# Kernel tuning notes

Measured on AMD Instinct MI355X. Metric: run time of the kernel, lower is better.

The kernel has to match this reference:

```python
import jax, jax.numpy as jnp
import numpy as np

N_NODES = 100000
N_EDGES = 1600000
D_INPUT = 128
D_HIDDEN = 16
N_HEADS = 8
NCLASSES = 40
N_GRAPHS = 64
ALPHA = 0.2  # LeakyReLU negative slope
INIT = 0.01  # GAT_param_init uniform range


def setup_inputs() -> dict:
    key = jax.random.key(0)
    ks = jax.random.split(key, 7)
    x = jax.random.normal(ks[0], (N_NODES, D_INPUT), dtype=jnp.float32)
    edge_idx = jax.random.randint(ks[1], (2, N_EDGES), 0, N_NODES, dtype=jnp.int64)
    batch = jnp.sort(jax.random.randint(ks[2], (N_NODES,), 0, N_GRAPHS, dtype=jnp.int64))
    # layer1: d_input -> n_heads * d_hidden, concat aggregate
    W1 = jax.random.uniform(ks[3], (D_INPUT, N_HEADS * D_HIDDEN), dtype=jnp.float32, minval=-INIT, maxval=INIT)
    a1 = jax.random.uniform(ks[4], (N_HEADS, 2 * D_HIDDEN), dtype=jnp.float32, minval=-INIT, maxval=INIT)
    # layer2: n_heads*d_hidden -> nclasses, 1 head, mean aggregate
    W2 = jax.random.uniform(ks[5], (N_HEADS * D_HIDDEN, NCLASSES), dtype=jnp.float32, minval=-INIT, maxval=INIT)
    a2 = jax.random.uniform(ks[6], (1, 2 * NCLASSES), dtype=jnp.float32, minval=-INIT, maxval=INIT)
    return {"x": x, "W1": W1, "a1": a1, "W2": W2, "a2": a2, "edge_idx": edge_idx, "batch": batch}


def _gat_layer(x, W, a, n_heads, d_out, src, dst, aggregate):
    # x: [N, d_in]; W: [d_in, H*D]; a: [H, 2*D]
    n = x.shape[0]
    Wh = (x @ W).reshape(n, n_heads, d_out)                  # [N, H, D]
    e_src = jnp.einsum('nhd,hd->nh', Wh, a[:, :d_out])       # [N, H]
    e_dst = jnp.einsum('nhd,hd->nh', Wh, a[:, d_out:])       # [N, H]
    e = jax.nn.leaky_relu(e_src[src] + e_dst[dst], ALPHA)    # [E, H]
    # segment softmax over edges sharing the same destination node
    m = jax.ops.segment_max(e, dst, num_segments=n)          # [N, H]
    m = jnp.where(jnp.isfinite(m), m, 0.0)                   # nodes w/o in-edges
    ex = jnp.exp(e - m[dst])
    s = jax.ops.segment_sum(ex, dst, num_segments=n)
    att = ex / (s[dst] + 1e-16)                              # [E, H]
    # weighted scatter-aggregate of neighbor features
    out = jax.ops.segment_sum(att[:, :, None] * Wh[src], dst, num_segments=n)  # [N, H, D]
    if aggregate == 'concat':
        return out.reshape(n, n_heads * d_out)
    return out.mean(axis=1)


def reference(x, W1, a1, W2, a2, edge_idx, batch):
    # eval mode: F.dropout(training=False) is identity
    src, dst = edge_idx[0], edge_idx[1]
    h1 = _gat_layer(x, W1, a1, N_HEADS, D_HIDDEN, src, dst, 'concat')
    h1 = jax.nn.elu(h1)
    h2 = _gat_layer(h1, W2, a2, 1, NCLASSES, src, dst, 'mean')   # [N, nclasses]
    # global_mean_pool over graph ids
    sums = jax.ops.segment_sum(h2, batch, num_segments=N_GRAPHS)
    cnt = jax.ops.segment_sum(jnp.ones((h2.shape[0],), h2.dtype), batch, num_segments=N_GRAPHS)
    return sums / jnp.maximum(cnt, 1.0)[:, None]
```

## Files before the change

### kernel.cpp

```cpp
#include <hip/hip_runtime.h>
#include <hip/hip_bf16.h>

typedef unsigned short u16;
typedef unsigned int   u32;
typedef float f32x2 __attribute__((ext_vector_type(2)));
typedef float f32x4 __attribute__((ext_vector_type(4)));
typedef short bf16x8 __attribute__((ext_vector_type(8)));

static constexpr int NN = 100000;
static constexpr int NE = 1600000;
static constexpr int NG = 64;

static constexpr int BSH   = 8;
static constexpr int NBUCK = 391;
static constexpr int BCAP  = 5120;
static constexpr int PB    = 8;

__device__ __forceinline__ u16 bf16rte(float a) {
  u32 u = __builtin_bit_cast(u32, a);
  u = (u + 0x7FFFu + ((u >> 16) & 1u)) >> 16;
  return (u16)u;
}
__device__ __forceinline__ u32 bf16pair(float a, float b) {
  return (u32)bf16rte(a) | ((u32)bf16rte(b) << 16);
}
__device__ __forceinline__ float bflo(u32 u) { return __builtin_bit_cast(float, u << 16); }
__device__ __forceinline__ float bfhi(u32 u) { return __builtin_bit_cast(float, u & 0xFFFF0000u); }

__device__ __forceinline__ void pkfma(f32x2& a, f32x2 w2, u32 u) {
  f32x2 v;
  v.x = bflo(u); v.y = bfhi(u);
  asm("v_pk_fma_f32 %0, %1, %2, %0" : "+v"(a) : "v"(w2), "v"(v));
}

__global__ void k_prepW(const float* __restrict__ W1, u16* __restrict__ wsTg) {
  const int t = threadIdx.x;
  for (int rep = 0; rep < 64; ++rep) {
    int idx = rep * 256 + t;
    int k = idx >> 7, c = idx & 127;
    float v = W1[idx];
    wsTg[c * 128 + (((k >> 3) ^ (c & 7)) << 3) + (k & 7)] = bf16rte(v);
  }
}

__global__ __launch_bounds__(256) void k_gemm1(
    const float* __restrict__ x, const u16* __restrict__ wsTg, const float* __restrict__ a1,
    u16* __restrict__ Wh1b, float* __restrict__ es1, float* __restrict__ ed1)
{
  __shared__ u16 wsT[128][128];
  __shared__ u16 xsb[64][32];
  const int t = threadIdx.x;
  const int w = t >> 6, l = t & 63;
  const int rowBase = blockIdx.x * 64;

  {
    const uint4* src = (const uint4*)wsTg;
    uint4* dst = (uint4*)&wsT[0][0];
#pragma unroll
    for (int i = 0; i < 8; ++i) dst[t * 8 + i] = src[t * 8 + i];
  }

  f32x4 acc[4][2];
#pragma unroll
  for (int r = 0; r < 4; ++r)
#pragma unroll
    for (int cf = 0; cf < 2; ++cf) acc[r][cf] = (f32x4){0.f, 0.f, 0.f, 0.f};

  const int rr = t >> 2, cg = t & 3;
  const int grow_s = rowBase + rr;

  for (int kk0 = 0; kk0 < 128; kk0 += 32) {
    float4 v0 = make_float4(0.f, 0.f, 0.f, 0.f), v1 = v0;
    if (grow_s < NN) {
      v0 = *(const float4*)(&x[(size_t)grow_s * 128 + kk0 + cg * 8]);
      v1 = *(const float4*)(&x[(size_t)grow_s * 128 + kk0 + cg * 8 + 4]);
    }
    if (kk0) __syncthreads();
    {
      u32 p0 = bf16pair(v0.x, v0.y);
      u32 p1 = bf16pair(v0.z, v0.w);
      u32 p2 = bf16pair(v1.x, v1.y);
      u32 p3 = bf16pair(v1.z, v1.w);
      int sg = cg ^ ((rr >> 1) & 3);
      *(uint4*)(&xsb[rr][sg * 8]) = make_uint4(p0, p1, p2, p3);
    }
    __syncthreads();

    bf16x8 bfr[2];
#pragma unroll
    for (int cf = 0; cf < 2; ++cf) {
      int col = w * 32 + cf * 16 + (l & 15);
      int kg = (kk0 >> 3) + (l >> 4);
      bfr[cf] = *(const bf16x8*)(&wsT[col][(kg ^ (col & 7)) * 8]);
    }
#pragma unroll
    for (int r = 0; r < 4; ++r) {
      int row = r * 16 + (l & 15);
      int kg = l >> 4;
      bf16x8 afr = *(const bf16x8*)(&xsb[row][(kg ^ ((row >> 1) & 3)) * 8]);
#pragma unroll
      for (int cf = 0; cf < 2; ++cf)
        acc[r][cf] = __builtin_amdgcn_mfma_f32_16x16x32_bf16(afr, bfr[cf], acc[r][cf], 0, 0, 0);
    }
  }

  const int cl = l & 15;
  const int rq = l >> 4;
#pragma unroll
  for (int cf = 0; cf < 2; ++cf) {
    const int h = w * 2 + cf;
    const int gcol = w * 32 + cf * 16 + cl;
    const float as = a1[h * 32 + cl];
    const float ad = a1[h * 32 + 16 + cl];
#pragma unroll
    for (int r = 0; r < 4; ++r) {
#pragma unroll
      for (int i = 0; i < 4; ++i) {
        int grow = rowBase + r * 16 + rq * 4 + i;
        float wh = acc[r][cf][i];
        float ps = wh * as, pd = wh * ad;
        ps += __shfl_xor(ps, 1); ps += __shfl_xor(ps, 2);
        ps += __shfl_xor(ps, 4); ps += __shfl_xor(ps, 8);
        pd += __shfl_xor(pd, 1); pd += __shfl_xor(pd, 2);
        pd += __shfl_xor(pd, 4); pd += __shfl_xor(pd, 8);
        if (grow < NN) {
          Wh1b[(size_t)grow * 128 + gcol] = bf16rte(wh);
          if (cl == 0) { es1[grow * 8 + h] = ps; ed1[grow * 8 + h] = pd; }
        }
      }
    }
  }
}

__global__ __launch_bounds__(256) void k_bin(
    const int* __restrict__ src, const int* __restrict__ dst,
    int* __restrict__ cur, u32* __restrict__ ebuf)
{
  __shared__ int lcnt[512];
  __shared__ int goff[NBUCK];
  __shared__ u32 bin[4096];
  const int t = threadIdx.x;
  const int e0 = blockIdx.x * 4096;

  lcnt[t] = 0; lcnt[t + 256] = 0;
  __syncthreads();

  u32 ent[16]; short bb[16], lp[16];
#pragma unroll
  for (int i = 0; i < 16; ++i) {
    int e = e0 + i * 256 + t;
    if (e < NE) {
      int s = src[e], d = dst[e];
      int b = d >> BSH;
      ent[i] = (u32)s | ((u32)(d & 255) << 20);
      bb[i] = (short)b;
      lp[i] = (short)atomicAdd(&lcnt[b], 1);
    } else bb[i] = -1;
  }
  __syncthreads();
  for (int d = 1; d < 512; d <<= 1) {
    int v0 = (t >= d) ? lcnt[t - d] : 0;
    int v1 = (t + 256 >= d) ? lcnt[t + 256 - d] : 0;
    __syncthreads();
    lcnt[t] += v0; lcnt[t + 256] += v1;
    __syncthreads();
  }
  for (int b = t; b < NBUCK; b += 256) {
    int excl = b ? lcnt[b - 1] : 0;
    int cnt = lcnt[b] - excl;
    if (cnt) goff[b] = b * BCAP + atomicAdd(&cur[b], cnt);
  }
#pragma unroll
  for (int i = 0; i < 16; ++i) {
    if (bb[i] >= 0) {
      int excl = bb[i] ? lcnt[bb[i] - 1] : 0;
      bin[excl + lp[i]] = ent[i];
    }
  }
  __syncthreads();
  const int total = lcnt[NBUCK - 1];
  for (int i = t; i < total; i += 256) {
    int lo = 0, hi = NBUCK - 1;
    while (lo < hi) { int mid = (lo + hi) >> 1; if (lcnt[mid] > i) hi = mid; else lo = mid + 1; }
    int excl = lo ? lcnt[lo - 1] : 0;
    int g = goff[lo] + (i - excl);
    if (g < (lo + 1) * BCAP) ebuf[g] = bin[i];
  }
}

__global__ __launch_bounds__(256) void k_sort(
    const int* __restrict__ cur, u32* __restrict__ ebuf,
    int* __restrict__ offs, int* __restrict__ deg)
{
  __shared__ u32 ein[BCAP];
  __shared__ u32 eout[BCAP];
  __shared__ int nd[256];
  __shared__ int ncur[256];
  const int t = threadIdx.x;
  const int b = blockIdx.x;
  const int base = b * BCAP;
  int cnt = cur[b];
  if (cnt > BCAP) cnt = BCAP;
  const int nloc = min(256, NN - (b << BSH));

  for (int i = t; i < cnt; i += 256) ein[i] = ebuf[base + i];
  nd[t] = 0;
  __syncthreads();
  for (int i = t; i < cnt; i += 256) atomicAdd(&nd[ein[i] >> 20], 1);
  __syncthreads();
  const int myCnt = nd[t];
  for (int d = 1; d < 256; d <<= 1) {
    int v = (t >= d) ? nd[t - d] : 0;
    __syncthreads();
    nd[t] += v;
    __syncthreads();
  }
  const int excl = t ? nd[t - 1] : 0;
  ncur[t] = excl;
  if (t < nloc) {
    int node = (b << BSH) + t;
    offs[node] = base + excl;
    deg[node]  = myCnt;
  }
  __syncthreads();
  for (int i = t; i < cnt; i += 256) {
    u32 v = ein[i];
    int pos = atomicAdd(&ncur[v >> 20], 1);
    eout[pos] = v & 0xFFFFFu;
  }
  __syncthreads();
  for (int i = t; i < cnt; i += 256) ebuf[base + i] = eout[i];
}

__global__ __launch_bounds__(256) void k_agg1(
    const u16* __restrict__ Wh1b, const float* __restrict__ es1, const float* __restrict__ ed1,
    const int* __restrict__ offs, const int* __restrict__ deg, const int* __restrict__ csr,
    u16* __restrict__ h1b)
{
  const int wid = threadIdx.x >> 6;
  const int lane = threadIdx.x & 63;
  const int n = blockIdx.x * 4 + wid;
  if (n >= NN) return;
  const int s0 = offs[n];
  const int nE = deg[n];
  const int g = lane >> 4;
  const int db = lane & 15;
  const int h = db >> 1;
  const float edv = ed1[n * 8 + h];

  f32x2 acc[4];
#pragma unroll
  for (int i = 0; i < 4; ++i) { acc[i].x = 0.f; acc[i].y = 0.f; }
  float ssum = 0.f;

  int c0 = 0;
  for (; c0 + 16 <= nE; c0 += 16) {
    int ss[4];
#pragma unroll
    for (int q = 0; q < 4; ++q) ss[q] = csr[s0 + c0 + q * 4 + g];
    float zz[4];
#pragma unroll
    for (int q = 0; q < 4; ++q) {
      float z = es1[ss[q] * 8 + h] + edv;
      zz[q] = (z > 0.f) ? z : 0.2f * z;
    }
    uint4 raw[4];
#pragma unroll
    for (int q = 0; q < 4; ++q)
      raw[q] = *(const uint4*)(Wh1b + (size_t)ss[q] * 128 + db * 8);
#pragma unroll
    for (int q = 0; q < 4; ++q) {
      const float ww = __expf(zz[q]);
      ssum += ww;
      f32x2 w2; w2.x = ww; w2.y = ww;
      pkfma(acc[0], w2, raw[q].x);
      pkfma(acc[1], w2, raw[q].y);
      pkfma(acc[2], w2, raw[q].z);
      pkfma(acc[3], w2, raw[q].w);
    }
  }
  if (c0 < nE) {
    int jj[4], ss[4];
#pragma unroll
    for (int q = 0; q < 4; ++q) {
      jj[q] = c0 + q * 4 + g;
      ss[q] = csr[s0 + (jj[q] < nE ? jj[q] : 0)];
    }
    float zz[4];
#pragma unroll
    for (int q = 0; q < 4; ++q) {
      float z = es1[ss[q] * 8 + h] + edv;
      zz[q] = (z > 0.f) ? z : 0.2f * z;
    }
#pragma unroll
    for (int q = 0; q < 4; ++q) {
      if (jj[q] < nE) {
        const uint4 raw = *(const uint4*)(Wh1b + (size_t)ss[q] * 128 + db * 8);
        const float ww = __expf(zz[q]);
        ssum += ww;
        f32x2 w2; w2.x = ww; w2.y = ww;
        pkfma(acc[0], w2, raw.x);
        pkfma(acc[1], w2, raw.y);
        pkfma(acc[2], w2, raw.z);
        pkfma(acc[3], w2, raw.w);
      }
    }
  }
#pragma unroll
  for (int i = 0; i < 4; ++i) {
    acc[i].x += __shfl_xor(acc[i].x, 16);
    acc[i].y += __shfl_xor(acc[i].y, 16);
    acc[i].x += __shfl_xor(acc[i].x, 32);
    acc[i].y += __shfl_xor(acc[i].y, 32);
  }
  ssum += __shfl_xor(ssum, 16);
  ssum += __shfl_xor(ssum, 32);

  if (g == 0) {
    float inv = 1.f / (ssum + 1e-16f);
    float o[8];
#pragma unroll
    for (int i = 0; i < 4; ++i) {
      float v0 = acc[i].x * inv;
      float v1 = acc[i].y * inv;
      o[2 * i]     = (v0 > 0.f) ? v0 : expm1f(v0);
      o[2 * i + 1] = (v1 > 0.f) ? v1 : expm1f(v1);
    }
    u32 p0 = bf16pair(o[0], o[1]);
    u32 p1 = bf16pair(o[2], o[3]);
    u32 p2 = bf16pair(o[4], o[5]);
    u32 p3 = bf16pair(o[6], o[7]);
    *(uint4*)(h1b + (size_t)n * 128 + db * 8) = make_uint4(p0, p1, p2, p3);
  }
}

__global__ __launch_bounds__(256) void k_gemm2(
    const u16* __restrict__ h1b, const float* __restrict__ W2,
    const float* __restrict__ a2,
    u16* __restrict__ Wh2b, float* __restrict__ es2, float* __restrict__ ed2)
{
  __shared__ float hs[128][36];
  __shared__ float w2s[32][40];
  const int t = threadIdx.x;
  const int rowBase = blockIdx.x * 128;
  const int cg = t & 3;
  const int rs = t >> 2;
  float acc[2][10];
#pragma unroll
  for (int r = 0; r < 2; ++r)
#pragma unroll
    for (int j = 0; j < 10; ++j) acc[r][j] = 0.f;

  for (int k0 = 0; k0 < 128; k0 += 32) {
#pragma unroll
    for (int p = 0; p < 2; ++p) {
      int idx = (p * 256 + t) * 8;
      int rr = idx >> 5, cc = idx & 31;
      int grow = rowBase + rr;
      uint4 hv = make_uint4(0u, 0u, 0u, 0u);
      if (grow < NN) hv = *(const uint4*)(h1b + (size_t)grow * 128 + k0 + cc);
      float2* dst = (float2*)&hs[rr][cc];
      dst[0] = make_float2(bflo(hv.x), bfhi(hv.x));
      dst[1] = make_float2(bflo(hv.y), bfhi(hv.y));
      dst[2] = make_float2(bflo(hv.z), bfhi(hv.z));
      dst[3] = make_float2(bflo(hv.w), bfhi(hv.w));
    }
#pragma unroll
    for (int p = 0; p < 5; ++p) {
      int idx = p * 256 + t;
      int kk = idx / 40, cc = idx % 40;
      w2s[kk][cc] = W2[(size_t)(k0 + kk) * 40 + cc];
    }
    __syncthreads();
#pragma unroll
    for (int k = 0; k < 32; ++k) {
      float a0 = hs[rs][k], a1v = hs[rs + 64][k];
#pragma unroll
      for (int j = 0; j < 10; ++j) {
        float b = w2s[k][cg * 10 + j];
        acc[0][j] = fmaf(a0, b, acc[0][j]);
        acc[1][j] = fmaf(a1v, b, acc[1][j]);
      }
    }
    __syncthreads();
  }
  float a2s[10], a2d[10];
#pragma unroll
  for (int j = 0; j < 10; ++j) {
    a2s[j] = a2[cg * 10 + j];
    a2d[j] = a2[40 + cg * 10 + j];
  }
#pragma unroll
  for (int rr = 0; rr < 2; ++rr) {
    int grow = rowBase + rs + rr * 64;
    float pes = 0.f, ped = 0.f;
#pragma unroll
    for (int j = 0; j < 10; ++j) {
      float v = acc[rr][j];
      pes = fmaf(v, a2s[j], pes);
      ped = fmaf(v, a2d[j], ped);
    }
    if (grow < NN) {
      u32* dst = (u32*)(Wh2b + (size_t)grow * 48 + cg * 10);
      dst[0] = bf16pair(acc[rr][0], acc[rr][1]);
      dst[1] = bf16pair(acc[rr][2], acc[rr][3]);
      dst[2] = bf16pair(acc[rr][4], acc[rr][5]);
      dst[3] = bf16pair(acc[rr][6], acc[rr][7]);
      dst[4] = bf16pair(acc[rr][8], acc[rr][9]);
    }
    pes += __shfl_xor(pes, 1); pes += __shfl_xor(pes, 2);
    ped += __shfl_xor(ped, 1); ped += __shfl_xor(ped, 2);
    if (cg == 0 && grow < NN) { es2[grow] = pes; ed2[grow] = ped; }
  }
}

__global__ __launch_bounds__(256) void k_agg2(
    const u16* __restrict__ Wh2b, const float* __restrict__ es2, const float* __restrict__ ed2,
    const int* __restrict__ offs, const int* __restrict__ deg, const int* __restrict__ csr,
    float* __restrict__ h2)
{
  __shared__ float red[4][64][9];
  const int wid = threadIdx.x >> 6;
  const int lane = threadIdx.x & 63;
  const int n = blockIdx.x * 4 + wid;
  if (n >= NN) return;
  const int s0 = offs[n];
  const int nE = deg[n];
  const float edv = ed2[n];
  const int e5 = lane / 5, r5 = lane - e5 * 5;
  const bool act = lane < 60;

  f32x2 acc[4];
#pragma unroll
  for (int i = 0; i < 4; ++i) { acc[i].x = 0.f; acc[i].y = 0.f; }
  float ssum = 0.f;

  for (int c0 = 0; c0 < nE; c0 += 24) {
    const int j0 = c0 + e5;
    const int j1 = c0 + 12 + e5;
    const int sA = csr[s0 + (j0 < nE ? j0 : 0)];
    const int sB = csr[s0 + (j1 < nE ? j1 : 0)];
    float zA = es2[sA] + edv;
    float zB = es2[sB] + edv;
    zA = (zA > 0.f) ? zA : 0.2f * zA;
    zB = (zB > 0.f) ? zB : 0.2f * zB;
    if (act && j0 < nE) {
      const uint4 raw = *(const uint4*)(Wh2b + (size_t)sA * 48 + r5 * 8);
      const float w = __expf(zA);
      ssum += w;
      f32x2 w2; w2.x = w; w2.y = w;
      pkfma(acc[0], w2, raw.x);
      pkfma(acc[1], w2, raw.y);
      pkfma(acc[2], w2, raw.z);
      pkfma(acc[3], w2, raw.w);
    }
    if (act && j1 < nE) {
      const uint4 raw = *(const uint4*)(Wh2b + (size_t)sB * 48 + r5 * 8);
      const float w = __expf(zB);
      ssum += w;
      f32x2 w2; w2.x = w; w2.y = w;
      pkfma(acc[0], w2, raw.x);
      pkfma(acc[1], w2, raw.y);
      pkfma(acc[2], w2, raw.z);
      pkfma(acc[3], w2, raw.w);
    }
  }
#pragma unroll
  for (int i = 0; i < 4; ++i) {
    red[wid][lane][2 * i]     = acc[i].x;
    red[wid][lane][2 * i + 1] = acc[i].y;
  }
  red[wid][lane][8] = ssum;
  __builtin_amdgcn_wave_barrier();
  if (lane < 40) {
    int slot = lane >> 3, i = lane & 7;
    float a = 0.f, sm = 0.f;
#pragma unroll
    for (int g = 0; g < 12; ++g) {
      a  += red[wid][g * 5 + slot][i];
      sm += red[wid][g * 5][8];
    }
    h2[(size_t)n * 40 + lane] = a / (sm + 1e-16f);
  }
}

__global__ void k_gbounds(const int* __restrict__ batch, int* __restrict__ gstart) {
  int g = threadIdx.x;
  if (g > NG) return;
  int lo = 0, hi = NN;
  while (lo < hi) { int mid = (lo + hi) >> 1; if (batch[mid] < g) lo = mid + 1; else hi = mid; }
  gstart[g] = lo;
}

__global__ __launch_bounds__(256) void k_pool1(
    const float* __restrict__ h2, const int* __restrict__ gstart,
    float* __restrict__ partial)
{
  __shared__ float lds[25][10][4];
  const int g = blockIdx.x >> 3;
  const int p = blockIdx.x & 7;
  const int t = threadIdx.x;
  const int s0 = gstart[g], s1 = gstart[g + 1];
  const int len = s1 - s0;
  const int chunk = (len + PB - 1) / PB;
  const int start = s0 + p * chunk;
  const int end = min(start + chunk, s1);
  const int slot = t / 10, q = t - slot * 10;
  float4 acc = make_float4(0.f, 0.f, 0.f, 0.f);
  if (slot < 25) {
    for (int n = start + slot; n < end; n += 25) {
      const float4 v = *(const float4*)(&h2[(size_t)n * 40 + q * 4]);
      acc.x += v.x; acc.y += v.y; acc.z += v.z; acc.w += v.w;
    }
    lds[slot][q][0] = acc.x; lds[slot][q][1] = acc.y;
    lds[slot][q][2] = acc.z; lds[slot][q][3] = acc.w;
  }
  __syncthreads();
  if (t < 40) {
    const int qq = t >> 2, e = t & 3;
    float s = 0.f;
#pragma unroll
    for (int sl = 0; sl < 25; ++sl) s += lds[sl][qq][e];
    partial[(size_t)blockIdx.x * 40 + t] = s;
  }
}

__global__ void k_pool2(const float* __restrict__ partial, const int* __restrict__ gstart,
                        float* __restrict__ out)
{
  const int g = blockIdx.x;
  const int d = threadIdx.x;
  if (d >= 40) return;
  float s = 0.f;
#pragma unroll
  for (int p = 0; p < PB; ++p) s += partial[(size_t)(g * PB + p) * 40 + d];
  int cnt = gstart[g + 1] - gstart[g];
  if (cnt < 1) cnt = 1;
  out[g * 40 + d] = s / (float)cnt;
}

extern "C" void kernel_launch(void* const* d_in, const int* in_sizes, int n_in,
                              void* d_out, int out_size, void* d_ws, size_t ws_size,
                              hipStream_t stream)
{
  const float* x   = (const float*)d_in[0];
  const float* W1  = (const float*)d_in[1];
  const float* a1  = (const float*)d_in[2];
  const float* W2  = (const float*)d_in[3];
  const float* a2  = (const float*)d_in[4];
  const int* eidx  = (const int*)d_in[5];
  const int* batch = (const int*)d_in[6];
  float* out = (float*)d_out;

  char* ws = (char*)d_ws;
  u16*   Wh1b = (u16*)(ws + 0);
  u16*   Wh2b = (u16*)(ws + 0);
  float* h2   = (float*)(ws + 9600000);
  u16*   h1b  = (u16*)(ws + 25600000);
  float* es1  = (float*)(ws + 51200000);
  float* ed1  = (float*)(ws + 54400000);
  float* es2  = (float*)(ws + 57600000);
  float* ed2  = (float*)(ws + 58000000);
  u32*   ebuf = (u32*)(ws + 58400000);
  int*   offs = (int*)(ws + 66407680);
  int*   deg  = (int*)(ws + 66807680);
  int*   cur  = (int*)(ws + 67207680);
  int*   gstart = (int*)(ws + 67209728);
  float* partial = (float*)(ws + 67210240);
  u16*   wsTg = (u16*)(ws + 67292160);

  const int* esrc = eidx;
  const int* edst = eidx + NE;

  hipMemsetAsync(cur, 0, NBUCK * sizeof(int), stream);
  k_prepW<<<1, 256, 0, stream>>>(W1, wsTg);
  k_gbounds<<<1, 128, 0, stream>>>(batch, gstart);
  k_gemm1<<<(NN + 63) / 64, 256, 0, stream>>>(x, wsTg, a1, Wh1b, es1, ed1);
  k_bin<<<(NE + 4095) / 4096, 256, 0, stream>>>(esrc, edst, cur, ebuf);
  k_sort<<<NBUCK, 256, 0, stream>>>(cur, ebuf, offs, deg);
  k_agg1<<<(NN + 3) / 4, 256, 0, stream>>>(Wh1b, es1, ed1, offs, deg, (const int*)ebuf, h1b);
  k_gemm2<<<(NN + 127) / 128, 256, 0, stream>>>(h1b, W2, a2, Wh2b, es2, ed2);
  k_agg2<<<(NN + 3) / 4, 256, 0, stream>>>(Wh2b, es2, ed2, offs, deg, (const int*)ebuf, h2);
  k_pool1<<<NG * PB, 256, 0, stream>>>(h2, gstart, partial);
  k_pool2<<<NG, 64, 0, stream>>>(partial, gstart, out);
}
```

Before: 266.9 us.

## Merge prep kernels, add occupancy hints, remap agg2 lanes to 6 edges

Merges the W1 bf16 transpose and the graph-boundary binary search into one 65-block launch, which removes a kernel launch and spreads the weight prep across many blocks instead of one. Adds a minimum-occupancy hint of 8 to both aggregation kernels' launch bounds to cap register use. Changes layer-2 aggregation so each edge is split over 10 lanes reading 4 bf16 values each, with 6 edges per pass and 4 passes per chunk, so all CSR and score loads are issued before the feature gathers. This shrinks the LDS reduction from 12 to 6 partial groups, but the gathers are narrower (8-byte) loads.

After: 256.8 us. -3.8%, faster.

```diff
diff --git a/kernel.cpp b/kernel.cpp
--- a/kernel.cpp
+++ b/kernel.cpp
@@ -33,13 +33,20 @@
   asm("v_pk_fma_f32 %0, %1, %2, %0" : "+v"(a) : "v"(w2), "v"(v));
 }
 
-__global__ void k_prepW(const float* __restrict__ W1, u16* __restrict__ wsTg) {
-  const int t = threadIdx.x;
-  for (int rep = 0; rep < 64; ++rep) {
-    int idx = rep * 256 + t;
+__global__ void k_prep(const float* __restrict__ W1, u16* __restrict__ wsTg,
+                       const int* __restrict__ batch, int* __restrict__ gstart) {
+  const int bid = blockIdx.x;
+  if (bid < 64) {
+    int idx = bid * 256 + threadIdx.x;
     int k = idx >> 7, c = idx & 127;
-    float v = W1[idx];
-    wsTg[c * 128 + (((k >> 3) ^ (c & 7)) << 3) + (k & 7)] = bf16rte(v);
+    wsTg[c * 128 + (((k >> 3) ^ (c & 7)) << 3) + (k & 7)] = bf16rte(W1[idx]);
+  } else {
+    int g = threadIdx.x;
+    if (g <= NG) {
+      int lo = 0, hi = NN;
+      while (lo < hi) { int mid = (lo + hi) >> 1; if (batch[mid] < g) lo = mid + 1; else hi = mid; }
+      gstart[g] = lo;
+    }
   }
 }
 
@@ -232,7 +239,7 @@
   for (int i = t; i < cnt; i += 256) ebuf[base + i] = eout[i];
 }
 
-__global__ __launch_bounds__(256) void k_agg1(
+__global__ __launch_bounds__(256, 8) void k_agg1(
     const u16* __restrict__ Wh1b, const float* __restrict__ es1, const float* __restrict__ ed1,
     const int* __restrict__ offs, const int* __restrict__ deg, const int* __restrict__ csr,
     u16* __restrict__ h1b)
@@ -414,12 +421,12 @@
   }
 }
 
-__global__ __launch_bounds__(256) void k_agg2(
+__global__ __launch_bounds__(256, 8) void k_agg2(
     const u16* __restrict__ Wh2b, const float* __restrict__ es2, const float* __restrict__ ed2,
     const int* __restrict__ offs, const int* __restrict__ deg, const int* __restrict__ csr,
     float* __restrict__ h2)
 {
-  __shared__ float red[4][64][9];
+  __shared__ float red[4][64][5];
   const int wid = threadIdx.x >> 6;
   const int lane = threadIdx.x & 63;
   const int n = blockIdx.x * 4 + wid;
@@ -427,69 +434,54 @@
   const int s0 = offs[n];
   const int nE = deg[n];
   const float edv = ed2[n];
-  const int e5 = lane / 5, r5 = lane - e5 * 5;
+  int e6 = lane / 10;
+  const int r10 = lane - e6 * 10;
   const bool act = lane < 60;
-
-  f32x2 acc[4];
-#pragma unroll
-  for (int i = 0; i < 4; ++i) { acc[i].x = 0.f; acc[i].y = 0.f; }
+  if (e6 > 5) e6 = 5;
+
+  f32x2 acc0, acc1;
+  acc0.x = acc0.y = acc1.x = acc1.y = 0.f;
   float ssum = 0.f;
 
   for (int c0 = 0; c0 < nE; c0 += 24) {
-    const int j0 = c0 + e5;
-    const int j1 = c0 + 12 + e5;
-    const int sA = csr[s0 + (j0 < nE ? j0 : 0)];
-    const int sB = csr[s0 + (j1 < nE ? j1 : 0)];
-    float zA = es2[sA] + edv;
-    float zB = es2[sB] + edv;
-    zA = (zA > 0.f) ? zA : 0.2f * zA;
-    zB = (zB > 0.f) ? zB : 0.2f * zB;
-    if (act && j0 < nE) {
-      const uint4 raw = *(const uint4*)(Wh2b + (size_t)sA * 48 + r5 * 8);
-      const float w = __expf(zA);
-      ssum += w;
-      f32x2 w2; w2.x = w; w2.y = w;
-      pkfma(acc[0], w2, raw.x);
-      pkfma(acc[1], w2, raw.y);
-      pkfma(acc[2], w2, raw.z);
-      pkfma(acc[3], w2, raw.w);
-    }
-    if (act && j1 < nE) {
-      const uint4 raw = *(const uint4*)(Wh2b + (size_t)sB * 48 + r5 * 8);
-      const float w = __expf(zB);
-      ssum += w;
-      f32x2 w2; w2.x = w; w2.y = w;
-      pkfma(acc[0], w2, raw.x);
-      pkfma(acc[1], w2, raw.y);
-      pkfma(acc[2], w2, raw.z);
-      pkfma(acc[3], w2, raw.w);
-    }
-  }
-#pragma unroll
-  for (int i = 0; i < 4; ++i) {
-    red[wid][lane][2 * i]     = acc[i].x;
-    red[wid][lane][2 * i + 1] = acc[i].y;
-  }
-  red[wid][lane][8] = ssum;
+    int jj[4], ss[4];
+#pragma unroll
+    for (int q = 0; q < 4; ++q) {
+      jj[q] = c0 + q * 6 + e6;
+      ss[q] = csr[s0 + (jj[q] < nE ? jj[q] : 0)];
+    }
+    float zz[4];
+#pragma unroll
+    for (int q = 0; q < 4; ++q) {
+      float z = es2[ss[q]] + edv;
+      zz[q] = (z > 0.f) ? z : 0.2f * z;
+    }
+#pragma unroll
+    for (int q = 0; q < 4; ++q) {
+      if (act && jj[q] < nE) {
+        const uint2 raw = *(const uint2*)(Wh2b + (size_t)ss[q] * 48 + r10 * 4);
+        const float ww = __expf(zz[q]);
+        ssum += ww;
+        f32x2 w2; w2.x = ww; w2.y = ww;
+        pkfma(acc0, w2, raw.x);
+        pkfma(acc1, w2, raw.y);
+      }
+    }
+  }
+  red[wid][lane][0] = acc0.x; red[wid][lane][1] = acc0.y;
+  red[wid][lane][2] = acc1.x; red[wid][lane][3] = acc1.y;
+  red[wid][lane][4] = ssum;
   __builtin_amdgcn_wave_barrier();
   if (lane < 40) {
-    int slot = lane >> 3, i = lane & 7;
+    const int rb = lane >> 2, e = lane & 3;
     float a = 0.f, sm = 0.f;
 #pragma unroll
-    for (int g = 0; g < 12; ++g) {
-      a  += red[wid][g * 5 + slot][i];
-      sm += red[wid][g * 5][8];
+    for (int g = 0; g < 6; ++g) {
+      a  += red[wid][g * 10 + rb][e];
+      sm += red[wid][g * 10][4];
     }
     h2[(size_t)n * 40 + lane] = a / (sm + 1e-16f);
   }
-}
-
-__global__ void k_gbounds(const int* __restrict__ batch, int* __restrict__ gstart) {
-  int g = threadIdx.x;
-  if (g > NG) return;
-  int lo = 0, hi = NN;
-  while (lo < hi) { int mid = (lo + hi) >> 1; if (batch[mid] < g) lo = mid + 1; else hi = mid; }
-  gstart[g] = lo;
 }
 
 __global__ __launch_bounds__(256) void k_pool1(
@@ -573,8 +565,7 @@
   const int* edst = eidx + NE;
 
   hipMemsetAsync(cur, 0, NBUCK * sizeof(int), stream);
-  k_prepW<<<1, 256, 0, stream>>>(W1, wsTg);
-  k_gbounds<<<1, 128, 0, stream>>>(batch, gstart);
+  k_prep<<<65, 256, 0, stream>>>(W1, wsTg, batch, gstart);
   k_gemm1<<<(NN + 63) / 64, 256, 0, stream>>>(x, wsTg, a1, Wh1b, es1, ed1);
   k_bin<<<(NE + 4095) / 4096, 256, 0, stream>>>(esrc, edst, cur, ebuf);
   k_sort<<<NBUCK, 256, 0, stream>>>(cur, ebuf, offs, deg);
```
